# Optimization experiments

Measured on AMD Instinct MI355X. Metric: run time of the kernel, lower is better.

The kernel has to match this reference:

```python
import jax, jax.numpy as jnp
import numpy as np

EPS = 1e-6
HEADS = 8
DIM_HEAD = 64
SCALE = 16.0
DIM = 1024
INNER = HEADS * DIM_HEAD


def _l2norm(t):
    return t / jnp.clip(jnp.linalg.norm(t, axis=-1, keepdims=True), 1e-12)


def setup_inputs() -> dict:
    key = jax.random.key(0)
    k1, k2, k3, k4 = jax.random.split(key, 4)
    b, n = 2, 4096
    x = jax.random.normal(k1, (b, n, DIM), dtype=jnp.float32)
    # weights stored as [in, out] so application is x @ W
    Wq = jax.random.normal(k2, (DIM, INNER), dtype=jnp.float32) * 0.02
    Wkv = jax.random.normal(k3, (DIM, 2 * INNER), dtype=jnp.float32) * 0.02
    Wo = jax.random.normal(k4, (INNER, DIM), dtype=jnp.float32) * 0.02
    return {"x": x, "Wq": Wq, "Wkv": Wkv, "Wo": Wo}


def reference(x, Wq, Wkv, Wo):
    b, n, _ = x.shape
    q = (x @ Wq).reshape(b, n, HEADS, DIM_HEAD).transpose(0, 2, 1, 3)  # b h n d
    kv = x @ Wkv
    k = kv[..., :INNER].reshape(b, n, HEADS, DIM_HEAD).transpose(0, 2, 1, 3)
    v = kv[..., INNER:].reshape(b, n, HEADS, DIM_HEAD).transpose(0, 2, 1, 3)
    q = _l2norm(q)
    k = _l2norm(k)
    # cosine-sim attention: logits = scale * (q.k) - scale, logits <= 0 so exp is stable
    logits = jnp.einsum('bhid,bhjd->bhij', q, k) * SCALE - SCALE
    p = jnp.exp(logits)
    row_sums = jnp.clip(p.sum(axis=-1, keepdims=True), EPS)  # matches per-block EPS clamp in dense case
    out = jnp.einsum('bhij,bhjd->bhid', p, v) / row_sums  # b h n d
    out = out.transpose(0, 2, 1, 3).reshape(b, n, INNER)
    return out @ Wo
```

## Files before the change

kernel.cpp:

```cpp
#include <hip/hip_runtime.h>


typedef _Float16 f16;
typedef _Float16 f16x4 __attribute__((ext_vector_type(4)));
typedef _Float16 f16x8 __attribute__((ext_vector_type(8)));
typedef float f32x4 __attribute__((ext_vector_type(4)));
typedef float f32x16 __attribute__((ext_vector_type(16)));
typedef int i32x4 __attribute__((ext_vector_type(4)));

#define MFMA_F16(a, b, c) __builtin_amdgcn_mfma_f32_16x16x32_f16((a), (b), (c), 0, 0, 0)
#define MFMA32(a, b, c) __builtin_amdgcn_mfma_f32_32x32x16_f16((a), (b), (c), 0, 0, 0)

#define QSCALE 23.083120654223414f
#define EXPBIAS -9.083120654223414f

__device__ __forceinline__ void gl_lds16(const void* g, void* l) {
  __builtin_amdgcn_global_load_lds(
      (const __attribute__((address_space(1))) void*)g,
      (__attribute__((address_space(3))) void*)l, 16, 0, 0);
}

__global__ void convert_x_kernel(const float* __restrict__ x, f16* __restrict__ xh, int n8) {
  int i = blockIdx.x * 256 + threadIdx.x;
  if (i >= n8) return;
  const float4* xv = (const float4*)x;
  float4 a = xv[2 * i], b = xv[2 * i + 1];
  f16x8 o;
  o[0] = (f16)a.x; o[1] = (f16)a.y; o[2] = (f16)a.z; o[3] = (f16)a.w;
  o[4] = (f16)b.x; o[5] = (f16)b.y; o[6] = (f16)b.z; o[7] = (f16)b.w;
  ((f16x8*)xh)[i] = o;
}

__global__ void transpose_all_kernel(const float* __restrict__ Wq,
                                     const float* __restrict__ Wkv,
                                     const float* __restrict__ Wo,
                                     f16* __restrict__ Wqkv_t, f16* __restrict__ Wo_t) {
  __shared__ float t[64][65];
  const int z = blockIdx.z;
  const float* W; int ldw, col0, K, nc; f16* out;
  if (z == 0)      { W = Wq;  ldw = 512;  col0 = 0;   K = 1024; nc = 8;  out = Wqkv_t; }
  else if (z == 1) { W = Wkv; ldw = 1024; col0 = 0;   K = 1024; nc = 8;  out = Wqkv_t + 512 * 1024; }
  else if (z == 2) { W = Wkv; ldw = 1024; col0 = 512; K = 1024; nc = 8;  out = Wqkv_t + 1024 * 1024; }
  else             { W = Wo;  ldw = 1024; col0 = 0;   K = 512;  nc = 16; out = Wo_t; }
  if ((int)blockIdx.x >= nc || (int)blockIdx.y >= (K >> 6)) return;
  int tx = threadIdx.x, ty = threadIdx.y;
  int c0 = blockIdx.x * 64, k0 = blockIdx.y * 64;
#pragma unroll
  for (int i = 0; i < 8; i++)
    t[ty + i * 8][tx] = W[(long)(k0 + ty + i * 8) * ldw + col0 + c0 + tx];
  __syncthreads();
#pragma unroll
  for (int i = 0; i < 8; i++)
    out[(long)(c0 + ty + i * 8) * K + k0 + tx] = (f16)t[tx][ty + i * 8];
}

__global__ void transpose_v_kernel(const f16* __restrict__ Vb, f16* __restrict__ Vt, int n) {
  __shared__ f16 t[64 * 64];
  const int tid = threadIdx.x;
  const int bh = blockIdx.y;
  const int n0 = blockIdx.x * 64;
  const f16* src = Vb + ((long)bh * n + n0) * 64;
  const int j = tid >> 3, c = tid & 7;
  f16x8 v0 = *(const f16x8*)(src + j * 64 + c * 8);
  f16x8 v1 = *(const f16x8*)(src + (j + 32) * 64 + c * 8);
  *(f16x8*)(&t[j * 64 + ((c ^ (j & 7)) << 3)]) = v0;
  *(f16x8*)(&t[(j + 32) * 64 + ((c ^ (j & 7)) << 3)]) = v1;
  __syncthreads();
  const int d = tid >> 3, cj = tid & 7;
  f16x8 o0, o1;
#pragma unroll
  for (int e = 0; e < 8; e++) {
    int jj = cj * 8 + e;
    o0[e] = t[jj * 64 + (((d >> 3) ^ (jj & 7)) << 3) + (d & 7)];
    o1[e] = t[jj * 64 + ((((d + 32) >> 3) ^ (jj & 7)) << 3) + ((d + 32) & 7)];
  }
  *(f16x8*)(Vt + ((long)bh * 64 + d) * n + n0 + cj * 8) = o0;
  *(f16x8*)(Vt + ((long)bh * 64 + d + 32) * n + n0 + cj * 8) = o1;
}

template <int MODE>
__global__ __launch_bounds__(256, 2)
void gemm_kernel(const f16* __restrict__ A, const f16* __restrict__ Bt,
                 float* __restrict__ C,
                 f16* __restrict__ Qb, f16* __restrict__ Kb, f16* __restrict__ Vb,
                 int M, int N, int K) {
  __shared__ f16 As[128 * 32];
  __shared__ f16 Bs[128 * 32];
  const int tid = threadIdx.x;
  const int lane = tid & 63;
  const int wid = tid >> 6;
  const int wr = wid >> 1, wc = wid & 1;
  const int lr = lane & 15, lk = lane >> 4;
  const int lin = blockIdx.x;
  const int bx = ((lin & 7) << 3) | ((lin >> 3) & 7);
  const int by = lin >> 6;
  const long m0 = (long)bx * 128;
  const int n0 = by * 128;

  f32x4 acc[4][4] = {};

  const int c0 = tid, c1 = tid + 256;
  const int ar0 = c0 >> 2, ah0 = (c0 & 3) ^ ((ar0 >> 1) & 3);
  const int ar1 = c1 >> 2, ah1 = (c1 & 3) ^ ((ar1 >> 1) & 3);
  const f16* pa0 = A + (m0 + ar0) * K + ah0 * 8;
  const f16* pa1 = A + (m0 + ar1) * K + ah1 * 8;
  const f16* pb0 = Bt + (long)(n0 + ar0) * K + ah0 * 8;
  const f16* pb1 = Bt + (long)(n0 + ar1) * K + ah1 * 8;

  for (int k0 = 0; k0 < K; k0 += 32) {
    __syncthreads();
    gl_lds16(pa0 + k0, As + c0 * 8);
    gl_lds16(pa1 + k0, As + c1 * 8);
    gl_lds16(pb0 + k0, Bs + c0 * 8);
    gl_lds16(pb1 + k0, Bs + c1 * 8);
    __syncthreads();

    f16x8 af[4], bf[4];
#pragma unroll
    for (int mi = 0; mi < 4; mi++) {
      int row = wr * 64 + mi * 16 + lr;
      int ch = lk ^ ((row >> 1) & 3);
      af[mi] = *(const f16x8*)(As + row * 32 + ch * 8);
    }
#pragma unroll
    for (int ni = 0; ni < 4; ni++) {
      int row = wc * 64 + ni * 16 + lr;
      int ch = lk ^ ((row >> 1) & 3);
      bf[ni] = *(const f16x8*)(Bs + row * 32 + ch * 8);
    }
    __builtin_amdgcn_s_setprio(1);
#pragma unroll
    for (int mi = 0; mi < 4; mi++)
#pragma unroll
      for (int ni = 0; ni < 4; ni++)
        acc[mi][ni] = MFMA_F16(af[mi], bf[ni], acc[mi][ni]);
    __builtin_amdgcn_s_setprio(0);
  }

  if (MODE == 0) {
#pragma unroll
    for (int mi = 0; mi < 4; mi++) {
      long mrow = m0 + wr * 64 + mi * 16 + lk * 4;
#pragma unroll
      for (int r = 0; r < 4; r++)
#pragma unroll
        for (int ni = 0; ni < 4; ni++)
          C[(mrow + r) * N + n0 + wc * 64 + ni * 16 + lr] = acc[mi][ni][r];
    }
  } else {
    const int region = by >> 2;
    const int head = (by & 3) * 2 + wc;
    f16* buf = (region == 0) ? Qb : ((region == 1) ? Kb : Vb);
    const float nscale = (region == 0) ? QSCALE : 1.f;
#pragma unroll
    for (int mi = 0; mi < 4; mi++) {
      float scl[4];
      if (region < 2) {
#pragma unroll
        for (int r = 0; r < 4; r++) {
          float s2 = 0.f;
#pragma unroll
          for (int ni = 0; ni < 4; ni++) s2 += acc[mi][ni][r] * acc[mi][ni][r];
          s2 += __shfl_xor(s2, 1);
          s2 += __shfl_xor(s2, 2);
          s2 += __shfl_xor(s2, 4);
          s2 += __shfl_xor(s2, 8);
          scl[r] = nscale / fmaxf(sqrtf(s2), 1e-12f);
        }
      } else {
#pragma unroll
        for (int r = 0; r < 4; r++) scl[r] = 1.f;
      }
#pragma unroll
      for (int r = 0; r < 4; r++) {
        int m = (int)m0 + wr * 64 + mi * 16 + lk * 4 + r;
        int bb = m >> 12, nn = m & 4095;
        f16* dst = buf + (((long)(bb * 8 + head) * 4096 + nn) << 6);
#pragma unroll
        for (int ni = 0; ni < 4; ni++)
          dst[ni * 16 + lr] = (f16)(acc[mi][ni][r] * scl[r]);
      }
    }
  }
}

__global__ __launch_bounds__(256, 2)
void attn_kernel(const f16* __restrict__ Qb, const f16* __restrict__ Kb,
                 const f16* __restrict__ Vt, f16* __restrict__ Ob, int n) {
  __shared__ f16 Ks[2][128 * 64];
  __shared__ f16 Vs[2][64 * 128];
  const int tid = threadIdx.x, lane = tid & 63, wid = tid >> 6;
  const int ql = lane & 31, hi = lane >> 5;
  const int lin = blockIdx.x;
  const int bh = (lin & 7) | ((lin >> 8) << 3);
  const int qx = (lin >> 3) & 31;
  const long nl = n;
  const f16* Qg = Qb + (long)bh * nl * 64;
  const f16* Kg = Kb + (long)bh * nl * 64;
  const f16* Vg = Vt + (long)bh * 64 * nl;
  const int q0w = qx * 128 + wid * 32;

  f16x8 qf[4];
#pragma unroll
  for (int kc = 0; kc < 4; kc++)
    qf[kc] = *(const f16x8*)(Qg + (long)(q0w + ql) * 64 + kc * 16 + hi * 8);

  int ksrc[4], vsrc[4];
#pragma unroll
  for (int p = 0; p < 4; p++) {
    const int ci = tid + p * 256;
    const int kj = ci >> 3, kc_ = ci & 7;
    ksrc[p] = kj * 64 + ((kc_ ^ (kj & 7)) << 3);
    const int vd = ci >> 4, vc = ci & 15;
    vsrc[p] = vd * n + ((vc ^ (vd & 15)) << 3);
  }

  f32x16 oacc[2][2] = {};
  float rsum0 = 0.f, rsum1 = 0.f;
  f32x16 initv;
#pragma unroll
  for (int e = 0; e < 16; e++) initv[e] = EXPBIAS;
  const auto one2 = __builtin_amdgcn_cvt_pkrtz(1.f, 1.f);

#pragma unroll
  for (int p = 0; p < 4; p++) {
    gl_lds16(Kg + ksrc[p], &Ks[0][(tid + p * 256) * 8]);
    gl_lds16(Vg + vsrc[p], &Vs[0][(tid + p * 256) * 8]);
  }
  __syncthreads();

  const int nt = n >> 7;
  for (int t = 0; t < nt; t++) {
    const int cur = t & 1;
    if (t + 1 < nt) {
      const long kadv = (long)(t + 1) * 8192;
      const long vadv = (long)(t + 1) * 128;
#pragma unroll
      for (int p = 0; p < 4; p++) {
        gl_lds16(Kg + kadv + ksrc[p], &Ks[cur ^ 1][(tid + p * 256) * 8]);
        gl_lds16(Vg + vadv + vsrc[p], &Vs[cur ^ 1][(tid + p * 256) * 8]);
      }
    }

    f32x16 s_cur, s_nxt;
    {
      const int j = ql, sw = j & 7;
      __builtin_amdgcn_s_setprio(1);
      const f16x8 k0 = *(const f16x8*)(&Ks[cur][j * 64 + ((hi ^ sw) << 3)]);
      s_cur = MFMA32(k0, qf[0], initv);
#pragma unroll
      for (int kc = 1; kc < 4; kc++) {
        const f16x8 kf = *(const f16x8*)(&Ks[cur][j * 64 + ((((kc << 1) | hi) ^ sw) << 3)]);
        s_cur = MFMA32(kf, qf[kc], s_cur);
      }
      __builtin_amdgcn_s_setprio(0);
    }

#pragma unroll
    for (int jt = 0; jt < 4; jt++) {
      if (jt < 3) {
        const int j = (jt + 1) * 32 + ql, sw = j & 7;
        const f16x8 k0 = *(const f16x8*)(&Ks[cur][j * 64 + ((hi ^ sw) << 3)]);
        s_nxt = MFMA32(k0, qf[0], initv);
#pragma unroll
        for (int kc = 1; kc < 4; kc++) {
          const f16x8 kf = *(const f16x8*)(&Ks[cur][j * 64 + ((((kc << 1) | hi) ^ sw) << 3)]);
          s_nxt = MFMA32(kf, qf[kc], s_nxt);
        }
      }

      int w[8];
#pragma unroll
      for (int m = 0; m < 8; m++) {
        const float pa = __builtin_amdgcn_exp2f(s_cur[2 * m]);
        const float pb = __builtin_amdgcn_exp2f(s_cur[2 * m + 1]);
        const auto h = __builtin_amdgcn_cvt_pkrtz(pa, pb);
        if (m & 1)
          rsum1 = __builtin_amdgcn_fdot2(h, one2, rsum1, false);
        else
          rsum0 = __builtin_amdgcn_fdot2(h, one2, rsum0, false);
        w[m] = __builtin_bit_cast(int, h);
      }
#pragma unroll
      for (int kl = 0; kl < 2; kl++) {
        int a0 = w[4 * kl + 0], a1 = w[4 * kl + 1];
        int a2 = w[4 * kl + 2], a3 = w[4 * kl + 3];
        asm volatile("v_permlane32_swap_b32 %0, %1" : "+v"(a0), "+v"(a2));
        asm volatile("v_permlane32_swap_b32 %0, %1" : "+v"(a1), "+v"(a3));
        i32x4 fi = {a0, a1, a2, a3};
        const f16x8 pfrag = __builtin_bit_cast(f16x8, fi);
        const int kb = jt * 2 + kl;
        __builtin_amdgcn_s_setprio(1);
#pragma unroll
        for (int dt = 0; dt < 2; dt++) {
          const int d = dt * 32 + ql;
          const f16x8 vf =
              *(const f16x8*)(&Vs[cur][d * 128 + ((((kb << 1) | hi) ^ (d & 15)) << 3)]);
          oacc[kl][dt] = MFMA32(pfrag, vf, oacc[kl][dt]);
        }
        __builtin_amdgcn_s_setprio(0);
      }
      if (jt < 3) s_cur = s_nxt;
    }

    __syncthreads();
  }

  float rsum = rsum0 + rsum1;
  rsum += __shfl_xor(rsum, 32);
  const int bb = bh >> 3, hh = bh & 7;
#pragma unroll
  for (int r = 0; r < 16; r++) {
    const int qloc = (r & 3) + 8 * (r >> 2) + 4 * hi;
    const float sm = __shfl(rsum, qloc);
    const float inv = 1.f / fmaxf(sm, 0.016384f);
    f16* dst = Ob + (((long)(bb * 4096 + q0w + qloc)) << 9) + hh * 64;
    dst[ql] = (f16)((oacc[0][0][r] + oacc[1][0][r]) * inv);
    dst[32 + ql] = (f16)((oacc[0][1][r] + oacc[1][1][r]) * inv);
  }
}

extern "C" void kernel_launch(void* const* d_in, const int* in_sizes, int n_in,
                              void* d_out, int out_size, void* d_ws, size_t ws_size,
                              hipStream_t stream) {
  const float* x   = (const float*)d_in[0];
  const float* Wq  = (const float*)d_in[1];
  const float* Wkv = (const float*)d_in[2];
  const float* Wo  = (const float*)d_in[3];
  float* out = (float*)d_out;

  char* ws = (char*)d_ws;
  f16* xh     = (f16*)(ws);
  f16* Wqkv_t = (f16*)(ws + 16777216);
  f16* Wo_t   = (f16*)(ws + 19922944);
  f16* Qb     = (f16*)(ws + 20971520);
  f16* Kb     = (f16*)(ws + 29360128);
  f16* Vb     = (f16*)(ws + 37748736);
  f16* At     = (f16*)(ws + 46137344);
  f16* Vt     = xh;

  convert_x_kernel<<<4096, 256, 0, stream>>>(x, xh, 1048576);

  transpose_all_kernel<<<dim3(16, 16, 4), dim3(64, 8), 0, stream>>>(Wq, Wkv, Wo, Wqkv_t, Wo_t);

  gemm_kernel<1><<<768, 256, 0, stream>>>(xh, Wqkv_t, nullptr, Qb, Kb, Vb,
                                          8192, 1536, 1024);
  transpose_v_kernel<<<dim3(64, 16), 256, 0, stream>>>(Vb, Vt, 4096);
  attn_kernel<<<512, 256, 0, stream>>>(Qb, Kb, Vt, At, 4096);
  gemm_kernel<0><<<512, 256, 0, stream>>>(At, Wo_t, out, nullptr, nullptr, nullptr,
                                          8192, 1024, 512);
}
```

Before: 155.5 us.

## Single-buffer V tile in attention to fit three blocks per CU

The V tile is now single-buffered and loaded at the start of each iteration, overlapping with the QK^T and softmax work. The P fragments for the whole 128-key tile are kept in registers and the PV MFMAs run after an extra barrier. Launch bounds on both the attention and GEMM kernels are raised from 2 to 3 blocks per CU to increase occupancy. The costs are an extra __syncthreads per tile, loss of the cross-tile V prefetch, tighter register budgets that may cause spills, and no more software pipelining of the next S tile.

Result: slower. 164.1 us (+5.5%).

```diff
diff --git a/kernel.cpp b/kernel.cpp
--- a/kernel.cpp
+++ b/kernel.cpp
@@ -79,7 +79,7 @@
 }
 
 template <int MODE>
-__global__ __launch_bounds__(256, 2)
+__global__ __launch_bounds__(256, 3)
 void gemm_kernel(const f16* __restrict__ A, const f16* __restrict__ Bt,
                  float* __restrict__ C,
                  f16* __restrict__ Qb, f16* __restrict__ Kb, f16* __restrict__ Vb,
@@ -184,11 +184,11 @@
   }
 }
 
-__global__ __launch_bounds__(256, 2)
+__global__ __launch_bounds__(256, 3)
 void attn_kernel(const f16* __restrict__ Qb, const f16* __restrict__ Kb,
                  const f16* __restrict__ Vt, f16* __restrict__ Ob, int n) {
   __shared__ f16 Ks[2][128 * 64];
-  __shared__ f16 Vs[2][64 * 128];
+  __shared__ f16 Vs[64 * 128];
   const int tid = threadIdx.x, lane = tid & 63, wid = tid >> 6;
   const int ql = lane & 31, hi = lane >> 5;
   const int lin = blockIdx.x;
@@ -223,10 +223,8 @@
   const auto one2 = __builtin_amdgcn_cvt_pkrtz(1.f, 1.f);
 
 #pragma unroll
-  for (int p = 0; p < 4; p++) {
+  for (int p = 0; p < 4; p++)
     gl_lds16(Kg + ksrc[p], &Ks[0][(tid + p * 256) * 8]);
-    gl_lds16(Vg + vsrc[p], &Vs[0][(tid + p * 256) * 8]);
-  }
   __syncthreads();
 
   const int nt = n >> 7;
@@ -234,46 +232,36 @@
     const int cur = t & 1;
     if (t + 1 < nt) {
       const long kadv = (long)(t + 1) * 8192;
-      const long vadv = (long)(t + 1) * 128;
-#pragma unroll
-      for (int p = 0; p < 4; p++) {
+#pragma unroll
+      for (int p = 0; p < 4; p++)
         gl_lds16(Kg + kadv + ksrc[p], &Ks[cur ^ 1][(tid + p * 256) * 8]);
-        gl_lds16(Vg + vadv + vsrc[p], &Vs[cur ^ 1][(tid + p * 256) * 8]);
-      }
-    }
-
-    f32x16 s_cur, s_nxt;
+    }
     {
-      const int j = ql, sw = j & 7;
+      const long vadv = (long)t * 128;
+#pragma unroll
+      for (int p = 0; p < 4; p++)
+        gl_lds16(Vg + vadv + vsrc[p], &Vs[(tid + p * 256) * 8]);
+    }
+
+    f16x8 pf[8];
+#pragma unroll
+    for (int jt = 0; jt < 4; jt++) {
+      const int j = jt * 32 + ql, sw = j & 7;
       __builtin_amdgcn_s_setprio(1);
       const f16x8 k0 = *(const f16x8*)(&Ks[cur][j * 64 + ((hi ^ sw) << 3)]);
-      s_cur = MFMA32(k0, qf[0], initv);
+      f32x16 s = MFMA32(k0, qf[0], initv);
 #pragma unroll
       for (int kc = 1; kc < 4; kc++) {
         const f16x8 kf = *(const f16x8*)(&Ks[cur][j * 64 + ((((kc << 1) | hi) ^ sw) << 3)]);
-        s_cur = MFMA32(kf, qf[kc], s_cur);
+        s = MFMA32(kf, qf[kc], s);
       }
       __builtin_amdgcn_s_setprio(0);
-    }
-
-#pragma unroll
-    for (int jt = 0; jt < 4; jt++) {
-      if (jt < 3) {
-        const int j = (jt + 1) * 32 + ql, sw = j & 7;
-        const f16x8 k0 = *(const f16x8*)(&Ks[cur][j * 64 + ((hi ^ sw) << 3)]);
-        s_nxt = MFMA32(k0, qf[0], initv);
-#pragma unroll
-        for (int kc = 1; kc < 4; kc++) {
-          const f16x8 kf = *(const f16x8*)(&Ks[cur][j * 64 + ((((kc << 1) | hi) ^ sw) << 3)]);
-          s_nxt = MFMA32(kf, qf[kc], s_nxt);
-        }
-      }
 
       int w[8];
 #pragma unroll
       for (int m = 0; m < 8; m++) {
-        const float pa = __builtin_amdgcn_exp2f(s_cur[2 * m]);
-        const float pb = __builtin_amdgcn_exp2f(s_cur[2 * m + 1]);
+        const float pa = __builtin_amdgcn_exp2f(s[2 * m]);
+        const float pb = __builtin_amdgcn_exp2f(s[2 * m + 1]);
         const auto h = __builtin_amdgcn_cvt_pkrtz(pa, pb);
         if (m & 1)
           rsum1 = __builtin_amdgcn_fdot2(h, one2, rsum1, false);
@@ -288,20 +276,24 @@
         asm volatile("v_permlane32_swap_b32 %0, %1" : "+v"(a0), "+v"(a2));
         asm volatile("v_permlane32_swap_b32 %0, %1" : "+v"(a1), "+v"(a3));
         i32x4 fi = {a0, a1, a2, a3};
-        const f16x8 pfrag = __builtin_bit_cast(f16x8, fi);
-        const int kb = jt * 2 + kl;
-        __builtin_amdgcn_s_setprio(1);
-#pragma unroll
-        for (int dt = 0; dt < 2; dt++) {
-          const int d = dt * 32 + ql;
-          const f16x8 vf =
-              *(const f16x8*)(&Vs[cur][d * 128 + ((((kb << 1) | hi) ^ (d & 15)) << 3)]);
-          oacc[kl][dt] = MFMA32(pfrag, vf, oacc[kl][dt]);
-        }
-        __builtin_amdgcn_s_setprio(0);
-      }
-      if (jt < 3) s_cur = s_nxt;
-    }
+        pf[jt * 2 + kl] = __builtin_bit_cast(f16x8, fi);
+      }
+    }
+
+    __syncthreads();
+
+    __builtin_amdgcn_s_setprio(1);
+#pragma unroll
+    for (int kb = 0; kb < 8; kb++) {
+#pragma unroll
+      for (int dt = 0; dt < 2; dt++) {
+        const int d = dt * 32 + ql;
+        const f16x8 vf =
+            *(const f16x8*)(&Vs[d * 128 + ((((kb << 1) | hi) ^ (d & 15)) << 3)]);
+        oacc[kb & 1][dt] = MFMA32(pf[kb], vf, oacc[kb & 1][dt]);
+      }
+    }
+    __builtin_amdgcn_s_setprio(0);
 
     __syncthreads();
   }
```
